# Kernel optimization log

Measured on AMD Instinct MI355X. Metric: run time of the kernel, lower is better.

The kernel has to match this reference:

```python
import jax, jax.numpy as jnp
import numpy as np

E, K, B = 64, 8, 32
IN_DIM, OUT_DIM = 1024, 1024


def setup_inputs() -> dict:
    key = jax.random.key(0)
    k1, k2, k3, k4, k5, k6 = jax.random.split(key, 6)
    return {
        "weight_probs": jax.random.uniform(k1, (B, K), dtype=jnp.float32),
        "bias_probs": jax.random.uniform(k2, (B, K), dtype=jnp.float32),
        "weight_indices": jax.random.randint(k3, (B, K), 0, E, dtype=jnp.int64),
        "bias_indices": jax.random.randint(k4, (B, K), 0, E, dtype=jnp.int64),
        # parameter banks: one linear layer's params per expert
        "weight_bank": jax.random.normal(k5, (E, OUT_DIM, IN_DIM), dtype=jnp.float32) * 0.02,
        "bias_bank": jax.random.normal(k6, (E, OUT_DIM), dtype=jnp.float32) * 0.02,
    }


def reference(weight_probs, bias_probs, weight_indices, bias_indices, weight_bank, bias_bank):
    # _select_parameters: gather per-(batch, top_k) expert params
    sel_w = weight_bank[weight_indices]          # [B, K, O, I]
    sel_b = bias_bank[bias_indices]              # [B, K, O]
    # _compute_mixture: probability-weighted sum over the top_k axis
    weight_mixture = jnp.einsum("bk,bkoi->boi", weight_probs, sel_w)  # [B, O, I]
    bias_mixture = jnp.einsum("bk,bko->bo", bias_probs, sel_b)        # [B, O]
    return weight_mixture, bias_mixture
```

## Files before the change

kernel.cpp:

```cpp
#include <hip/hip_runtime.h>
#include <hip/hip_bf16.h>


typedef __attribute__((ext_vector_type(8)))  short short8v;
typedef __attribute__((ext_vector_type(16))) float f32x16;

constexpr int E = 64;
constexpr int K = 8;
constexpr int B = 32;
constexpr int IN_DIM = 1024;
constexpr int OUT_DIM = 1024;

constexpr int NCOL     = OUT_DIM * IN_DIM;
constexpr int BLK      = 256;
constexpr int GRID     = 512;
constexpr int WAVES    = GRID * 4;
constexpr int CPW      = NCOL / WAVES;
constexpr int CSTEP    = 128;
constexpr int STEPS    = CPW / CSTEP;
constexpr int NRG      = STEPS * 4;
constexpr int WM_ELEMS = B * NCOL;
constexpr int OB4      = OUT_DIM / 4;

struct HL { short h; short l; };

__device__ __forceinline__ HL split_bf16(float x) {
    const __hip_bfloat16 hb = __float2bfloat16(x);
    const float          hf = __bfloat162float(hb);
    const __hip_bfloat16 lb = __float2bfloat16(x - hf);
    HL r;
    r.h = __builtin_bit_cast(short, hb);
    r.l = __builtin_bit_cast(short, lb);
    return r;
}

__global__ __launch_bounds__(BLK, 2) void ParameterMixture_86835648790543_kernel(
    const float* __restrict__ wprobs,
    const float* __restrict__ bprobs,
    const int*   __restrict__ widx,
    const int*   __restrict__ bidx,
    const float* __restrict__ wbank,
    const float* __restrict__ bbank,
    float*       __restrict__ out)
{
    const int bid  = blockIdx.x;
    const int t    = threadIdx.x;
    const int wv   = t >> 6;
    const int lane = t & 63;
    const int m    = lane & 31;
    const int kh   = (lane >> 5) * 8;
    const int cl   = lane & 31;

    if (bid < 32) {
        const int tt   = bid * BLK + t;
        const int b    = tt / OB4;
        const int off4 = tt % OB4;
        const float4* __restrict__ bb4 = (const float4*)bbank;
        float4 a4 = make_float4(0.f, 0.f, 0.f, 0.f);
#pragma unroll
        for (int k = 0; k < K; ++k) {
            const float p = bprobs[b * K + k];
            const int   e = bidx[b * K + k];
            const float4 v = bb4[e * OB4 + off4];
            a4.x += p * v.x; a4.y += p * v.y;
            a4.z += p * v.z; a4.w += p * v.w;
        }
        ((float4*)(out + WM_ELEMS))[tt] = a4;
    }

    float wp[K];
    int   wi[K];
#pragma unroll
    for (int k2 = 0; k2 < K; ++k2) {
        wp[k2] = wprobs[m * K + k2];
        wi[k2] = widx[m * K + k2];
    }
    short8v aH[4], aL[4];
#pragma unroll
    for (int s = 0; s < 4; ++s) {
#pragma unroll
        for (int j = 0; j < 8; ++j) {
            const int e = s * 16 + kh + j;
            float p = 0.f;
#pragma unroll
            for (int k2 = 0; k2 < K; ++k2)
                p += (wi[k2] == e) ? wp[k2] : 0.f;
            const HL r = split_bf16(p);
            aH[s][j] = r.h;
            aL[s][j] = r.l;
        }
    }

    const size_t ncol     = (size_t)NCOL;
    const int    wave_id  = bid * 4 + wv;
    const int    col_base = wave_id * CPW;

    auto load_rg = [&](float4 (&w)[8], int g) {
        if (g > NRG - 1) g = NRG - 1;
        const int c0 = col_base + (g >> 2) * CSTEP + 4 * cl;
        const int r0 = (g & 3) * 16 + kh;
        const float* __restrict__ base = wbank + c0;
#pragma unroll
        for (int j = 0; j < 8; ++j)
            w[j] = *(const float4*)(base + (size_t)(r0 + j) * ncol);
    };

    float4 bufA[8], bufB[8];
    load_rg(bufA, 0);
    load_rg(bufB, 1);

#pragma unroll 1
    for (int step = 0; step < STEPS; ++step) {
        f32x16 acc[4];
#pragma unroll
        for (int tt2 = 0; tt2 < 4; ++tt2)
#pragma unroll
            for (int i = 0; i < 16; ++i) acc[tt2][i] = 0.f;

        const int g0 = step * 4;

        auto compute_rg = [&](const float4 (&w)[8], int rg) {
            short8v bh[4], bl[4];
#pragma unroll
            for (int j = 0; j < 8; ++j) {
                const HL rx = split_bf16(w[j].x);
                const HL ry = split_bf16(w[j].y);
                const HL rz = split_bf16(w[j].z);
                const HL rw = split_bf16(w[j].w);
                bh[0][j] = rx.h; bl[0][j] = rx.l;
                bh[1][j] = ry.h; bl[1][j] = ry.l;
                bh[2][j] = rz.h; bl[2][j] = rz.l;
                bh[3][j] = rw.h; bl[3][j] = rw.l;
            }
#pragma unroll
            for (int tt2 = 0; tt2 < 4; ++tt2) {
                acc[tt2] = __builtin_amdgcn_mfma_f32_32x32x16_bf16(aH[rg], bh[tt2], acc[tt2], 0, 0, 0);
                acc[tt2] = __builtin_amdgcn_mfma_f32_32x32x16_bf16(aH[rg], bl[tt2], acc[tt2], 0, 0, 0);
                acc[tt2] = __builtin_amdgcn_mfma_f32_32x32x16_bf16(aL[rg], bh[tt2], acc[tt2], 0, 0, 0);
            }
        };

        compute_rg(bufA, 0);  load_rg(bufA, g0 + 2);
        compute_rg(bufB, 1);  load_rg(bufB, g0 + 3);
        compute_rg(bufA, 2);  load_rg(bufA, g0 + 4);
        compute_rg(bufB, 3);  load_rg(bufB, g0 + 5);

        const int c0 = col_base + step * CSTEP + 4 * cl;
        float* __restrict__ ob = out + c0 + (size_t)((lane >> 5) * 4) * ncol;
#pragma unroll
        for (int reg = 0; reg < 16; ++reg) {
            const int row = (reg & 3) + 8 * (reg >> 2);
            const float4 v = make_float4(acc[0][reg], acc[1][reg], acc[2][reg], acc[3][reg]);
            *(float4*)(ob + (size_t)row * ncol) = v;
        }
    }
}

extern "C" void kernel_launch(void* const* d_in, const int* in_sizes, int n_in,
                              void* d_out, int out_size, void* d_ws, size_t ws_size,
                              hipStream_t stream) {
    const float* wprobs = (const float*)d_in[0];
    const float* bprobs = (const float*)d_in[1];
    const int*   widx   = (const int*)d_in[2];
    const int*   bidx   = (const int*)d_in[3];
    const float* wbank  = (const float*)d_in[4];
    const float* bbank  = (const float*)d_in[5];
    float*       out    = (float*)d_out;

    ParameterMixture_86835648790543_kernel<<<GRID, BLK, 0, stream>>>(
        wprobs, bprobs, widx, bidx, wbank, bbank, out);
}
```

Baseline: 93.75 us.

## Stage weight bank tiles through LDS with async global_load_lds double buffering

Replaces per-wave register double-buffered float4 loads with block-cooperative asynchronous global-to-LDS loads into a two-buffer shared tile of 64 experts by 128 columns. Each block now owns a contiguous range of 16 tiles, and each wave computes one 32-column MFMA slice per tile. Stores become scalar per-lane rather than float4. The aim is to overlap memory latency with compute and reduce register pressure. The cost is extra barriers, LDS traffic, and narrower stores.

Result: slower. 105.5 us (+12.5%).

```diff
diff --git a/kernel.cpp b/kernel.cpp
--- a/kernel.cpp
+++ b/kernel.cpp
@@ -8,19 +8,19 @@
 constexpr int E = 64;
 constexpr int K = 8;
 constexpr int B = 32;
-constexpr int IN_DIM = 1024;
 constexpr int OUT_DIM = 1024;
 
-constexpr int NCOL     = OUT_DIM * IN_DIM;
+constexpr int NCOL     = 1024 * 1024;
 constexpr int BLK      = 256;
 constexpr int GRID     = 512;
-constexpr int WAVES    = GRID * 4;
-constexpr int CPW      = NCOL / WAVES;
-constexpr int CSTEP    = 128;
-constexpr int STEPS    = CPW / CSTEP;
-constexpr int NRG      = STEPS * 4;
+constexpr int TCOLS    = 128;
+constexpr int TILES    = 16;
+constexpr int CPB      = TCOLS * TILES;
 constexpr int WM_ELEMS = B * NCOL;
 constexpr int OB4      = OUT_DIM / 4;
+
+#define AS1C(p) ((const __attribute__((address_space(1))) void*)(p))
+#define AS3(p)  ((__attribute__((address_space(3))) void*)(p))
 
 struct HL { short h; short l; };
 
@@ -43,6 +43,8 @@
     const float* __restrict__ bbank,
     float*       __restrict__ out)
 {
+    __shared__ float sT[2][64][TCOLS];
+
     const int bid  = blockIdx.x;
     const int t    = threadIdx.x;
     const int wv   = t >> 6;
@@ -91,68 +93,70 @@
         }
     }
 
-    const size_t ncol     = (size_t)NCOL;
-    const int    wave_id  = bid * 4 + wv;
-    const int    col_base = wave_id * CPW;
+    const size_t ncol   = (size_t)NCOL;
+    const int    c_base = bid * CPB;
 
-    auto load_rg = [&](float4 (&w)[8], int g) {
-        if (g > NRG - 1) g = NRG - 1;
-        const int c0 = col_base + (g >> 2) * CSTEP + 4 * cl;
-        const int r0 = (g & 3) * 16 + kh;
-        const float* __restrict__ base = wbank + c0;
+    auto stage = [&](int buf, int i) {
+        const int c0 = c_base + i * TCOLS;
+        char* lds_base = (char*)&sT[buf][0][0];
 #pragma unroll
-        for (int j = 0; j < 8; ++j)
-            w[j] = *(const float4*)(base + (size_t)(r0 + j) * ncol);
+        for (int r = 0; r < 8; ++r) {
+            const int row = r * 8 + 2 * wv + (lane >> 5);
+            const float* src = wbank + (size_t)row * ncol + c0 + (lane & 31) * 4;
+            __builtin_amdgcn_global_load_lds(
+                (const __attribute__((address_space(1))) unsigned int*)AS1C(src),
+                (__attribute__((address_space(3))) unsigned int*)AS3(lds_base + r * 4096 + wv * 1024),
+                16, 0, 0);
+        }
     };
 
-    float4 bufA[8], bufB[8];
-    load_rg(bufA, 0);
-    load_rg(bufB, 1);
+    auto compute = [&](int buf, int i) {
+        const int c0 = c_base + i * TCOLS;
+        f32x16 acc;
+#pragma unroll
+        for (int q = 0; q < 16; ++q) acc[q] = 0.f;
 
-#pragma unroll 1
-    for (int step = 0; step < STEPS; ++step) {
-        f32x16 acc[4];
 #pragma unroll
-        for (int tt2 = 0; tt2 < 4; ++tt2)
-#pragma unroll
-            for (int i = 0; i < 16; ++i) acc[tt2][i] = 0.f;
-
-        const int g0 = step * 4;
-
-        auto compute_rg = [&](const float4 (&w)[8], int rg) {
-            short8v bh[4], bl[4];
+        for (int rg = 0; rg < 4; ++rg) {
+            short8v bh, bl;
 #pragma unroll
             for (int j = 0; j < 8; ++j) {
-                const HL rx = split_bf16(w[j].x);
-                const HL ry = split_bf16(w[j].y);
-                const HL rz = split_bf16(w[j].z);
-                const HL rw = split_bf16(w[j].w);
-                bh[0][j] = rx.h; bl[0][j] = rx.l;
-                bh[1][j] = ry.h; bl[1][j] = ry.l;
-                bh[2][j] = rz.h; bl[2][j] = rz.l;
-                bh[3][j] = rw.h; bl[3][j] = rw.l;
+                const float x = sT[buf][rg * 16 + kh + j][wv * 32 + cl];
+                const HL r = split_bf16(x);
+                bh[j] = r.h;
+                bl[j] = r.l;
             }
-#pragma unroll
-            for (int tt2 = 0; tt2 < 4; ++tt2) {
-                acc[tt2] = __builtin_amdgcn_mfma_f32_32x32x16_bf16(aH[rg], bh[tt2], acc[tt2], 0, 0, 0);
-                acc[tt2] = __builtin_amdgcn_mfma_f32_32x32x16_bf16(aH[rg], bl[tt2], acc[tt2], 0, 0, 0);
-                acc[tt2] = __builtin_amdgcn_mfma_f32_32x32x16_bf16(aL[rg], bh[tt2], acc[tt2], 0, 0, 0);
-            }
-        };
+            acc = __builtin_amdgcn_mfma_f32_32x32x16_bf16(aH[rg], bh, acc, 0, 0, 0);
+            acc = __builtin_amdgcn_mfma_f32_32x32x16_bf16(aH[rg], bl, acc, 0, 0, 0);
+            acc = __builtin_amdgcn_mfma_f32_32x32x16_bf16(aL[rg], bh, acc, 0, 0, 0);
+        }
 
-        compute_rg(bufA, 0);  load_rg(bufA, g0 + 2);
-        compute_rg(bufB, 1);  load_rg(bufB, g0 + 3);
-        compute_rg(bufA, 2);  load_rg(bufA, g0 + 4);
-        compute_rg(bufB, 3);  load_rg(bufB, g0 + 5);
-
-        const int c0 = col_base + step * CSTEP + 4 * cl;
-        float* __restrict__ ob = out + c0 + (size_t)((lane >> 5) * 4) * ncol;
+        float* __restrict__ ob = out + (size_t)(4 * (lane >> 5)) * ncol + c0 + wv * 32 + cl;
 #pragma unroll
         for (int reg = 0; reg < 16; ++reg) {
             const int row = (reg & 3) + 8 * (reg >> 2);
-            const float4 v = make_float4(acc[0][reg], acc[1][reg], acc[2][reg], acc[3][reg]);
-            *(float4*)(ob + (size_t)row * ncol) = v;
+            ob[(size_t)row * ncol] = acc[reg];
         }
+    };
+
+    stage(0, 0);
+    stage(1, 1);
+
+#pragma unroll 1
+    for (int i = 0; i < TILES; ++i) {
+        const int buf = i & 1;
+        if (i + 1 < TILES) {
+            asm volatile("s_waitcnt vmcnt(8)" ::: "memory");
+        } else {
+            asm volatile("s_waitcnt vmcnt(0)" ::: "memory");
+        }
+        __builtin_amdgcn_s_barrier();
+
+        compute(buf, i);
+
+        asm volatile("" ::: "memory");
+        __builtin_amdgcn_s_barrier();
+        if (i + 2 < TILES) stage(buf, i + 2);
     }
 }
 
```
